# Kernel optimization log

Hardware: AMD Instinct MI355X
Metric: run time of the kernel (lower is better)

The kernel has to match this reference:

```python
import jax, jax.numpy as jnp
import numpy as np

C_IN, C_OUT = 256, 128

def setup_inputs() -> dict:
    key = jax.random.key(0)
    k1, k2, k3, k4, k5, k6 = jax.random.split(key, 6)
    B, H, W = 8, 64, 64
    p = jax.random.normal(k1, (B, C_IN, H, W), dtype=jnp.float32)
    b = jax.random.normal(k2, (B, C_IN, H, W), dtype=jnp.float32)
    # 1x1 conv weights (Conv2d with kernel 1 == pointwise matmul) + biases
    sq = 1.0 / np.sqrt(C_IN)
    Wq = jax.random.uniform(k3, (C_OUT, C_IN), jnp.float32, -sq, sq)
    bq = jax.random.uniform(k4, (C_OUT,), jnp.float32, -sq, sq)
    Wk = jax.random.uniform(k5, (C_OUT, C_IN), jnp.float32, -sq, sq)
    bk = jax.random.uniform(k6, (C_OUT,), jnp.float32, -sq, sq)
    return {"p": p, "b": b, "Wq": Wq, "bq": bq, "Wk": Wk, "bk": bk}

def reference(p, b, Wq, bq, Wk, bk):
    B, C, H, W = p.shape
    N = H * W
    # 1x1 convs -> flatten spatial dim to N
    q = jnp.einsum('bchw,oc->bhwo', p, Wq) + bq          # [B,H,W,Co]
    q = q.reshape(B, N, -1).astype(jnp.float32)           # [B,N,Co] (query permuted)
    k = jnp.einsum('bchw,oc->bohw', b, Wk) + bk[None, :, None, None]
    k = k.reshape(B, -1, N).astype(jnp.float32)           # [B,Co,N]
    energy = jnp.einsum('bnc,bcm->bnm', q, k)             # [B,N,N] unscaled
    attention = jax.nn.softmax(energy, axis=-1)           # softmax over keys
    value = b.reshape(B, C, N)                            # [B,C,N]
    out = jnp.einsum('bnm,bcm->bcn', attention, value)    # [B,C,N]
    return out.reshape(B, C, H, W)
```

## Files before the change

### kernel.cpp

```cpp
#include <hip/hip_runtime.h>
#include <hip/hip_bf16.h>
#include <math.h>


#define B_   8
#define CIN  256
#define COUT 128
#define NN   4096

typedef _Float16 half8  __attribute__((ext_vector_type(8)));
typedef short    short8 __attribute__((ext_vector_type(8)));
typedef float    f32x4  __attribute__((ext_vector_type(4)));

#define LOG2E 1.44269504088896340736f

__device__ __forceinline__ unsigned short f2bf(float f) {
    union { float f; unsigned u; } v; v.f = f;
    return (unsigned short)((v.u + 0x7FFFu + ((v.u >> 16) & 1u)) >> 16);
}
__device__ __forceinline__ unsigned short f2h(float f) {
    union { _Float16 h; unsigned short u; } v; v.h = (_Float16)f;
    return v.u;
}
__device__ __forceinline__ unsigned int cvt_pk_bf16(float lo, float hi) {
    unsigned int r;
    asm("v_cvt_pk_bf16_f32 %0, %1, %2" : "=v"(r) : "v"(lo), "v"(hi));
    return r;
}
__device__ __forceinline__ float dpp_xor1(float x) {
    union { float f; int i; } u; u.f = x;
    u.i = __builtin_amdgcn_mov_dpp(u.i, 0xB1, 0xF, 0xF, true);
    return u.f;
}
__device__ __forceinline__ void dma16(void* lds, const void* g) {
    __builtin_amdgcn_global_load_lds(
        (const __attribute__((address_space(1))) unsigned int*)g,
        (__attribute__((address_space(3))) unsigned int*)lds,
        16, 0, 0);
}

__global__ __launch_bounds__(256) void cvt_w(const float* __restrict__ Wq,
                                             const float* __restrict__ Wk,
                                             const float* __restrict__ bq,
                                             _Float16* __restrict__ Whq,
                                             _Float16* __restrict__ Whk,
                                             float* __restrict__ bqs) {
    const int bx = blockIdx.x, t = threadIdx.x;
    const int isK = (bx >= 32);
    const float* src = isK ? Wk : Wq;
    _Float16* dst = isK ? Whk : Whq;
    const float scale = isK ? 1.0f : LOG2E;
    const int idx = (bx & 31) * 256 + t;
    float4 v = ((const float4*)src)[idx];
    unsigned long long pk = (unsigned long long)f2h(v.x * scale)
                          | ((unsigned long long)f2h(v.y * scale) << 16)
                          | ((unsigned long long)f2h(v.z * scale) << 32)
                          | ((unsigned long long)f2h(v.w * scale) << 48);
    ((unsigned long long*)dst)[idx] = pk;
    if (bx == 0 && t < COUT) bqs[t] = bq[t] * LOG2E;
}

__global__ __launch_bounds__(256) void proj3(const float* __restrict__ X,
                                             const _Float16* __restrict__ Wh,
                                             const float* __restrict__ bias,
                                             _Float16* __restrict__ outN,
                                             _Float16* __restrict__ outT,
                                             unsigned short* __restrict__ Vb)
{
    __shared__ __align__(16) unsigned short T[64 * 264];
    const int bx = blockIdx.x, b = bx >> 6, n0 = (bx & 63) << 6;
    const int t  = threadIdx.x;
    const int cr = t >> 2;
    const int nch = (t & 3) << 4;

#pragma unroll
    for (int it = 0; it < 4; ++it) {
        const int c = it * 64 + cr;
        const float* src = X + ((size_t)(b * CIN + c) * NN + n0 + nch);
        float v[16];
#pragma unroll
        for (int k = 0; k < 4; ++k) {
            float4 f = *(const float4*)(src + k * 4);
            v[k*4] = f.x; v[k*4+1] = f.y; v[k*4+2] = f.z; v[k*4+3] = f.w;
        }
#pragma unroll
        for (int j = 0; j < 16; ++j) T[(nch + j) * 264 + c] = f2h(v[j]);
        if (Vb) {
            unsigned short o[16];
#pragma unroll
            for (int j = 0; j < 16; ++j) o[j] = f2bf(v[j]);
            unsigned short* dst = Vb + (size_t)(b * CIN + c) * NN + n0 + nch;
            *(int4*)dst = *(int4*)o;
            *(int4*)(dst + 8) = *(int4*)(o + 8);
        }
    }
    __syncthreads();

    const int w = t >> 6, lane = t & 63, l15 = lane & 15, quad = lane >> 4, q8 = quad * 8;
    half8 a[8];
#pragma unroll
    for (int s = 0; s < 8; ++s)
        a[s] = *(const half8*)&T[(w * 16 + l15) * 264 + s * 32 + q8];
    f32x4 D[8];
#pragma unroll
    for (int og = 0; og < 8; ++og) D[og] = (f32x4){0.f, 0.f, 0.f, 0.f};
#pragma unroll
    for (int s = 0; s < 8; ++s) {
        const _Float16* wp = Wh + (size_t)l15 * CIN + s * 32 + q8;
#pragma unroll
        for (int og = 0; og < 8; ++og) {
            half8 wf = *(const half8*)(wp + og * 16 * CIN);
            D[og] = __builtin_amdgcn_mfma_f32_16x16x32_f16(a[s], wf, D[og], 0, 0, 0);
        }
    }
    const int nrow = n0 + w * 16 + quad * 4;
    if (outT) {
#pragma unroll
        for (int og = 0; og < 8; ++og) {
            const int o = og * 16 + l15;
            const float bo = bias[o];
            const int c = o >> 3, j = o & 7;
            const int sw = (c & 7) << 2;
#pragma unroll
            for (int r2 = 0; r2 < 4; ++r2) {
                const int n = nrow + r2;
                const int tile = n >> 5, m = n & 31;
                const size_t pos = ((size_t)(b * 128 + tile) * 512
                                    + c * 32 + ((m + sw) & 31)) * 8 + j;
                outT[pos] = (_Float16)(D[og][r2] + bo);
            }
        }
    } else {
#pragma unroll
        for (int og = 0; og < 8; ++og) {
            const int o = og * 16 + l15;
            const float bo = bias[o];
            _Float16* op = outN + ((size_t)(b * NN + nrow) * COUT + o);
#pragma unroll
            for (int r2 = 0; r2 < 4; ++r2)
                op[(size_t)r2 * COUT] = (_Float16)(D[og][r2] + bo);
        }
    }
}

__global__ __launch_bounds__(256, 2) void flash_kernel(const _Float16* __restrict__ Q,
                                                       const _Float16* __restrict__ Ktt,
                                                       const unsigned short* __restrict__ V,
                                                       float* __restrict__ out) {
    __shared__ __align__(16) _Float16       K0sh[32 * 128];
    __shared__ __align__(16) _Float16       K1sh[32 * 128];
    __shared__ __align__(16) unsigned short V0sh[256 * 32];
    __shared__ __align__(16) unsigned short V1sh[256 * 32];
    __shared__ __align__(16) unsigned short V2sh[256 * 32];
    __shared__ __align__(16) unsigned short P0sh[64 * 40];
    __shared__ __align__(16) unsigned short P1sh[64 * 40];
    __shared__ __align__(16) float          Lsh[64];

    const int bx   = blockIdx.x;
    const int b    = bx >> 6;
    const int q0   = (bx & 63) << 6;
    const int t    = threadIdx.x;
    const int w    = t >> 6;
    const int lane = t & 63;
    const int l15  = lane & 15;
    const int quad = lane >> 4;
    const int q8   = quad * 8;

    const _Float16* Qg = Q + (size_t)b * NN * COUT;
    const _Float16* Kb = Ktt + (size_t)b * 128 * 4096;
    const unsigned short* Vg = V + (size_t)b * CIN * NN;

    half8 Qf[4];
    {
        const _Float16* qr = Qg + (size_t)(q0 + w * 16 + l15) * COUT;
#pragma unroll
        for (int s = 0; s < 4; ++s)
            Qf[s] = *(const half8*)(qr + s * 32 + q8);
    }

    f32x4 O[16];
#pragma unroll
    for (int i = 0; i < 16; ++i) O[i] = (f32x4){0.f, 0.f, 0.f, 0.f};
    float lsum[4] = {0.f, 0.f, 0.f, 0.f};

    const int vmq   = ((lane & 3) - ((lane >> 3) & 3)) & 3;
    const int vcrow = lane >> 2;
    const int vslot = (quad + (l15 >> 1)) & 3;

    auto issueK = [&](int kt, _Float16* Kd) {
        const _Float16* gk = Kb + (size_t)kt * 4096;
        dma16(Kd + (w * 2 + 0) * 512, gk + (w * 2 + 0) * 512 + lane * 8);
        dma16(Kd + (w * 2 + 1) * 512, gk + (w * 2 + 1) * 512 + lane * 8);
    };
    auto issueV = [&](int kt, unsigned short* Vd) {
        const int k0 = kt << 5;
#pragma unroll
        for (int i = 0; i < 4; ++i) {
            const int cc = (w * 4 + i) * 16 + vcrow;
            dma16(Vd + (w * 4 + i) * 512,
                  Vg + (size_t)cc * NN + k0 + vmq * 8);
        }
    };

    auto halfstep = [&](int kt, const _Float16* Kc, _Float16* Kn,
                        const unsigned short* Va, unsigned short* Vn2,
                        unsigned short* Pc) {
        if (kt + 1 < 128) issueK(kt + 1, Kn);

        f32x4 S0 = {0.f, 0.f, 0.f, 0.f}, S1 = {0.f, 0.f, 0.f, 0.f};
        __builtin_amdgcn_s_setprio(1);
#pragma unroll
        for (int s = 0; s < 4; ++s) {
            const int kc = 4 * s + quad;
            const int sw = (kc & 7) << 2;
            const int x0 = (l15 + sw) & 31;
            half8 kf0 = *(const half8*)(Kc + (kc * 32 + x0) * 8);
            half8 kf1 = *(const half8*)(Kc + (kc * 32 + (x0 ^ 16)) * 8);
            S0 = __builtin_amdgcn_mfma_f32_16x16x32_f16(Qf[s], kf0, S0, 0, 0, 0);
            S1 = __builtin_amdgcn_mfma_f32_16x16x32_f16(Qf[s], kf1, S1, 0, 0, 0);
        }
        __builtin_amdgcn_s_setprio(0);

        f32x4 E0, E1;
#pragma unroll
        for (int r = 0; r < 4; ++r) {
            E0[r] = exp2f(S0[r]);
            E1[r] = exp2f(S1[r]);
            lsum[r] += E0[r] + E1[r];
        }
        {
            f32x4 P0, P1;
#pragma unroll
            for (int r = 0; r < 4; ++r) { P0[r] = dpp_xor1(E0[r]); P1[r] = dpp_xor1(E1[r]); }
            const int odd = l15 & 1;
            unsigned short* wp0 = Pc + w * 640
                                + (((quad << 2) + (odd << 1)) * 40) + (l15 & ~1);
            unsigned int pk0 = cvt_pk_bf16(odd ? P0[2] : E0[0], odd ? E0[2] : P0[0]);
            unsigned int pk1 = cvt_pk_bf16(odd ? P0[3] : E0[1], odd ? E0[3] : P0[1]);
            unsigned int pk2 = cvt_pk_bf16(odd ? P1[2] : E1[0], odd ? E1[2] : P1[0]);
            unsigned int pk3 = cvt_pk_bf16(odd ? P1[3] : E1[1], odd ? E1[3] : P1[1]);
            *(unsigned int*)&wp0[0]  = pk0;
            *(unsigned int*)&wp0[40] = pk1;
            *(unsigned int*)&wp0[16] = pk2;
            *(unsigned int*)&wp0[56] = pk3;
        }

        __syncthreads();

        if (kt + 2 < 128) issueV(kt + 2, Vn2);

        {
            short8 pf[4];
#pragma unroll
            for (int ni = 0; ni < 4; ++ni)
                pf[ni] = *(const short8*)(Pc + (ni * 16 + l15) * 40 + q8);
            const unsigned short* vb = Va + (w * 64 + l15) * 32 + vslot * 8;
            __builtin_amdgcn_s_setprio(1);
#pragma unroll
            for (int cj = 0; cj < 4; ++cj) {
                short8 vf = *(const short8*)(vb + cj * 512);
#pragma unroll
                for (int ni = 0; ni < 4; ++ni)
                    O[ni * 4 + cj] = __builtin_amdgcn_mfma_f32_16x16x32_bf16(pf[ni], vf, O[ni * 4 + cj], 0, 0, 0);
            }
            __builtin_amdgcn_s_setprio(0);
        }
    };

    issueK(0, K0sh);
    issueV(0, V0sh);
    issueV(1, V1sh);
    __syncthreads();

    _Float16*       Kc = K0sh; _Float16*       Kn = K1sh;
    unsigned short* Va = V0sh; unsigned short* Vm = V1sh; unsigned short* Vn2 = V2sh;
    unsigned short* Pc = P0sh; unsigned short* Pn = P1sh;
#pragma unroll 1
    for (int kt = 0; kt < 128; ++kt) {
        halfstep(kt, Kc, Kn, Va, Vn2, Pc);
        _Float16* tk = Kc; Kc = Kn; Kn = tk;
        unsigned short* tv = Va; Va = Vm; Vm = Vn2; Vn2 = tv;
        unsigned short* tp = Pc; Pc = Pn; Pn = tp;
    }

#pragma unroll
    for (int r = 0; r < 4; ++r) {
        float s = lsum[r];
        s += __shfl_xor(s, 1);
        s += __shfl_xor(s, 2);
        s += __shfl_xor(s, 4);
        s += __shfl_xor(s, 8);
        if (l15 == 0) Lsh[w * 16 + (quad << 2) + r] = s;
    }
    __syncthreads();
    float* ob = out + (size_t)b * CIN * NN + q0;
#pragma unroll
    for (int ni = 0; ni < 4; ++ni) {
        const f32x4 lv = *(const f32x4*)&Lsh[ni * 16 + (quad << 2)];
        f32x4 linv;
#pragma unroll
        for (int r = 0; r < 4; ++r) linv[r] = 1.0f / lv[r];
        const int nb = ni * 16 + (quad << 2);
#pragma unroll
        for (int cj = 0; cj < 4; ++cj) {
            const int c = w * 64 + cj * 16 + l15;
            f32x4 val = O[ni * 4 + cj];
#pragma unroll
            for (int r = 0; r < 4; ++r) val[r] *= linv[r];
            *(f32x4*)(ob + (size_t)c * NN + nb) = val;
        }
    }
}

extern "C" void kernel_launch(void* const* d_in, const int* in_sizes, int n_in,
                              void* d_out, int out_size, void* d_ws, size_t ws_size,
                              hipStream_t stream) {
    const float* p  = (const float*)d_in[0];
    const float* bv = (const float*)d_in[1];
    const float* Wq = (const float*)d_in[2];
    const float* bq = (const float*)d_in[3];
    const float* Wk = (const float*)d_in[4];
    const float* bk = (const float*)d_in[5];
    float* outp = (float*)d_out;

    char* ws = (char*)d_ws;
    const size_t szQ = (size_t)B_ * NN * COUT * 2;
    const size_t szV = (size_t)B_ * NN * CIN * 2;
    const size_t szW = (size_t)COUT * CIN * 2;
    _Float16*       Qh  = (_Float16*)ws;
    _Float16*       Ktt = (_Float16*)(ws + szQ);
    unsigned short* Vb  = (unsigned short*)(ws + 2 * szQ);
    _Float16*       Whq = (_Float16*)(ws + 2 * szQ + szV);
    _Float16*       Whk = (_Float16*)(ws + 2 * szQ + szV + szW);
    float*          bqs = (float*)(ws + 2 * szQ + szV + 2 * szW);

    cvt_w<<<64, 256, 0, stream>>>(Wq, Wk, bq, Whq, Whk, bqs);
    proj3<<<512, 256, 0, stream>>>(p,  Whq, bqs, Qh, (_Float16*)nullptr, (unsigned short*)nullptr);
    proj3<<<512, 256, 0, stream>>>(bv, Whk, bk,  (_Float16*)nullptr, Ktt, Vb);
    flash_kernel<<<512, 256, 0, stream>>>(Qh, Ktt, Vb, outp);
}
```

Baseline: 284.4 us.

## Restructure projection kernel: direct A loads, LDS-staged coalesced stores, prefetched weights

The projection kernel no longer transposes X through shared memory. Each lane now loads its MFMA A-fragment straight from global memory and converts it to f16 with round-toward-zero packing. Output tiles are staged in shared memory and written back as contiguous 16-byte vectors instead of scattered 2-byte stores, and weight fragments are double-buffered across the K loop. The V bf16 conversion uses the hardware packed convert. The trade-off is partially coalesced strided global reads for A and slightly different f16 rounding.

New measurement: 285.6 us. About the same (+0.4%).

```diff
diff --git a/kernel.cpp b/kernel.cpp
--- a/kernel.cpp
+++ b/kernel.cpp
@@ -14,10 +14,6 @@
 
 #define LOG2E 1.44269504088896340736f
 
-__device__ __forceinline__ unsigned short f2bf(float f) {
-    union { float f; unsigned u; } v; v.f = f;
-    return (unsigned short)((v.u + 0x7FFFu + ((v.u >> 16) & 1u)) >> 16);
-}
 __device__ __forceinline__ unsigned short f2h(float f) {
     union { _Float16 h; unsigned short u; } v; v.h = (_Float16)f;
     return v.u;
@@ -26,6 +22,12 @@
     unsigned int r;
     asm("v_cvt_pk_bf16_f32 %0, %1, %2" : "=v"(r) : "v"(lo), "v"(hi));
     return r;
+}
+__device__ __forceinline__ unsigned int pkrtz(float lo, float hi) {
+    typedef __fp16 fp16x2 __attribute__((ext_vector_type(2)));
+    union { fp16x2 h; unsigned int u; } c;
+    c.h = __builtin_amdgcn_cvt_pkrtz(lo, hi);
+    return c.u;
 }
 __device__ __forceinline__ float dpp_xor1(float x) {
     union { float f; int i; } u; u.f = x;
@@ -67,53 +69,70 @@
                                              _Float16* __restrict__ outT,
                                              unsigned short* __restrict__ Vb)
 {
-    __shared__ __align__(16) unsigned short T[64 * 264];
+    __shared__ __align__(16) unsigned short T[64 * 136];
     const int bx = blockIdx.x, b = bx >> 6, n0 = (bx & 63) << 6;
     const int t  = threadIdx.x;
-    const int cr = t >> 2;
-    const int nch = (t & 3) << 4;
-
-#pragma unroll
-    for (int it = 0; it < 4; ++it) {
-        const int c = it * 64 + cr;
-        const float* src = X + ((size_t)(b * CIN + c) * NN + n0 + nch);
-        float v[16];
-#pragma unroll
-        for (int k = 0; k < 4; ++k) {
-            float4 f = *(const float4*)(src + k * 4);
-            v[k*4] = f.x; v[k*4+1] = f.y; v[k*4+2] = f.z; v[k*4+3] = f.w;
-        }
-#pragma unroll
-        for (int j = 0; j < 16; ++j) T[(nch + j) * 264 + c] = f2h(v[j]);
-        if (Vb) {
-            unsigned short o[16];
-#pragma unroll
-            for (int j = 0; j < 16; ++j) o[j] = f2bf(v[j]);
+
+    if (Vb) {
+        const int cr = t >> 2;
+        const int nch = (t & 3) << 4;
+#pragma unroll
+        for (int it = 0; it < 4; ++it) {
+            const int c = it * 64 + cr;
+            const float* src = X + ((size_t)(b * CIN + c) * NN + n0 + nch);
+            unsigned int o2[8];
+#pragma unroll
+            for (int k = 0; k < 4; ++k) {
+                float4 f = *(const float4*)(src + k * 4);
+                o2[k * 2]     = cvt_pk_bf16(f.x, f.y);
+                o2[k * 2 + 1] = cvt_pk_bf16(f.z, f.w);
+            }
             unsigned short* dst = Vb + (size_t)(b * CIN + c) * NN + n0 + nch;
-            *(int4*)dst = *(int4*)o;
-            *(int4*)(dst + 8) = *(int4*)(o + 8);
-        }
-    }
-    __syncthreads();
+            *(int4*)dst = *(int4*)&o2[0];
+            *(int4*)(dst + 8) = *(int4*)&o2[4];
+        }
+    }
 
     const int w = t >> 6, lane = t & 63, l15 = lane & 15, quad = lane >> 4, q8 = quad * 8;
+
     half8 a[8];
-#pragma unroll
-    for (int s = 0; s < 8; ++s)
-        a[s] = *(const half8*)&T[(w * 16 + l15) * 264 + s * 32 + q8];
+    {
+        const float* Xa = X + ((size_t)(b * CIN + q8) * NN) + n0 + w * 16 + l15;
+#pragma unroll
+        for (int s = 0; s < 8; ++s) {
+            const float* xs = Xa + (size_t)s * 32 * NN;
+            float av[8];
+#pragma unroll
+            for (int j = 0; j < 8; ++j) av[j] = xs[(size_t)j * NN];
+            union { half8 h; unsigned int u[4]; } af;
+#pragma unroll
+            for (int j = 0; j < 4; ++j) af.u[j] = pkrtz(av[2 * j], av[2 * j + 1]);
+            a[s] = af.h;
+        }
+    }
+
     f32x4 D[8];
 #pragma unroll
     for (int og = 0; og < 8; ++og) D[og] = (f32x4){0.f, 0.f, 0.f, 0.f};
+    const _Float16* wbase = Wh + (size_t)l15 * CIN + q8;
+    half8 wf[2][8];
+#pragma unroll
+    for (int og = 0; og < 8; ++og)
+        wf[0][og] = *(const half8*)(wbase + og * 16 * CIN);
 #pragma unroll
     for (int s = 0; s < 8; ++s) {
-        const _Float16* wp = Wh + (size_t)l15 * CIN + s * 32 + q8;
-#pragma unroll
-        for (int og = 0; og < 8; ++og) {
-            half8 wf = *(const half8*)(wp + og * 16 * CIN);
-            D[og] = __builtin_amdgcn_mfma_f32_16x16x32_f16(a[s], wf, D[og], 0, 0, 0);
-        }
-    }
-    const int nrow = n0 + w * 16 + quad * 4;
+        if (s < 7) {
+            const _Float16* wp = wbase + (s + 1) * 32;
+#pragma unroll
+            for (int og = 0; og < 8; ++og)
+                wf[(s + 1) & 1][og] = *(const half8*)(wp + og * 16 * CIN);
+        }
+#pragma unroll
+        for (int og = 0; og < 8; ++og)
+            D[og] = __builtin_amdgcn_mfma_f32_16x16x32_f16(a[s], wf[s & 1][og], D[og], 0, 0, 0);
+    }
+
+    const int nrow = w * 16 + quad * 4;
     if (outT) {
 #pragma unroll
         for (int og = 0; og < 8; ++og) {
@@ -124,22 +143,32 @@
 #pragma unroll
             for (int r2 = 0; r2 < 4; ++r2) {
                 const int n = nrow + r2;
-                const int tile = n >> 5, m = n & 31;
-                const size_t pos = ((size_t)(b * 128 + tile) * 512
-                                    + c * 32 + ((m + sw) & 31)) * 8 + j;
-                outT[pos] = (_Float16)(D[og][r2] + bo);
+                const int tl = n >> 5, m = n & 31;
+                T[tl * 4096 + (c * 32 + ((m + sw) & 31)) * 8 + j] = f2h(D[og][r2] + bo);
             }
         }
+        __syncthreads();
+        _Float16* dstk = outT + ((size_t)(b * 128 + (n0 >> 5)) * 4096 + t * 32);
+        const unsigned short* srck = T + t * 32;
+#pragma unroll
+        for (int k = 0; k < 4; ++k)
+            ((int4*)dstk)[k] = ((const int4*)srck)[k];
     } else {
 #pragma unroll
         for (int og = 0; og < 8; ++og) {
             const int o = og * 16 + l15;
             const float bo = bias[o];
-            _Float16* op = outN + ((size_t)(b * NN + nrow) * COUT + o);
 #pragma unroll
             for (int r2 = 0; r2 < 4; ++r2)
-                op[(size_t)r2 * COUT] = (_Float16)(D[og][r2] + bo);
-        }
+                T[(nrow + r2) * 136 + o] = f2h(D[og][r2] + bo);
+        }
+        __syncthreads();
+        const int n = t >> 2, seg = t & 3;
+        const unsigned short* srcp = T + n * 136 + seg * 32;
+        _Float16* dstp = outN + ((size_t)(b * NN + n0 + n) * COUT + seg * 32);
+#pragma unroll
+        for (int k = 0; k < 4; ++k)
+            ((int4*)dstp)[k] = ((const int4*)srcp)[k];
     }
 }
 
```
